# Kernel tuning notes

Hardware: AMD Instinct MI355X
Metric: run time of the kernel (lower is better)

## Reference

```python
import jax, jax.numpy as jnp
import numpy as np

NHEAD = 8
TOPKS = (16, 8, 8)


def _to_tokens(x, nhead):
    # [b,c,h,w] -> [b, h*w, nhead, c//nhead]  (matches 'b c h w -> b (h w) c' then head split)
    b, c, h, w = x.shape
    return x.reshape(b, c, h * w).transpose(0, 2, 1).reshape(b, h * w, nhead, c // nhead)


def _gather_heads(table, idx):
    # table [b,S,nh,d], idx [b,L,K,nh] -> [b,L,K,nh,d]; per-head gather along S
    def per_b(tb, ib):
        return jax.vmap(lambda th, ih: th[ih], in_axes=(1, -1), out_axes=-2)(tb, ib)
    return jax.vmap(per_b)(table, idx)


def _coarse_level(q, k, v, topk, nhead):
    b, c, h, w = k.shape
    d = c // nhead
    qt, kt, vt = _to_tokens(q, nhead), _to_tokens(k, nhead), _to_tokens(v, nhead)
    QK = jnp.einsum('blhd,bshd->blsh', qt, kt) * (d ** -0.5)
    A = jax.nn.softmax(QK, axis=-2)  # softmax over source positions s
    _, ids = jax.lax.top_k(jnp.moveaxis(A, -2, -1), topk)  # top-k over s
    topk_idx = jnp.moveaxis(ids, -1, -2)  # [b, L, topk, nh]
    msg = jnp.einsum('blsh,bshd->blhd', A, vt)
    return msg, topk_idx


def _fine_level(q, k, v, topk_pos, topk_prev, topk, nhead):
    b, c, h0, w0 = q.shape
    _, _, h1, w1 = k.shape
    d = c // nhead
    kt, vt = _to_tokens(k, nhead), _to_tokens(v, nhead)
    # group queries into 2x2 quadrants: [b, (h0/2*w0/2), 4, nh, d]
    qg = q.reshape(b, c, h0 // 2, 2, w0 // 2, 2)
    qg = qg.transpose(0, 2, 4, 3, 5, 1).reshape(b, (h0 // 2) * (w0 // 2), 4, nhead, d)
    py, px = topk_pos[0] * 2, topk_pos[1] * 2  # [b, L, topk_prev, nh]
    # expand each coarse winner into its 4 children at this level
    idx = jnp.stack([(py + x) * w1 + (px + y) for x in (0, 1) for y in (0, 1)], axis=3)
    K = topk_prev * 4
    idx = idx.reshape(b, -1, K, nhead)  # [b, L, K, nh]
    gk = _gather_heads(kt, idx)  # [b, L, K, nh, d]  (score_computation_op gather)
    gv = _gather_heads(vt, idx)  # (value_aggregation_op gather)
    QK = jnp.einsum('blthd,blkhd->bltkh', qg, gk) * (d ** -0.5)
    A = jax.nn.softmax(QK, axis=-2)  # softmax over the K gathered keys
    _, ids = jax.lax.top_k(jnp.moveaxis(A, -2, -1), topk)
    tk_ids = jnp.moveaxis(ids, -1, -2)  # [b, L, 4, topk, nh]
    msg = jnp.einsum('bltkh,blkhd->blthd', A, gv)  # [b, L, 4, nh, d]
    idx_rep = jnp.broadcast_to(idx[:, :, None, :, :], A.shape)
    topk_idx = jnp.take_along_axis(idx_rep, tk_ids, axis=3)  # absolute source positions
    # 'b (h w) (t1 t2) k nh -> b (h t1 w t2) k nh'
    topk_idx = topk_idx.reshape(b, h0 // 2, w0 // 2, 2, 2, topk, nhead)
    topk_idx = topk_idx.transpose(0, 1, 3, 2, 4, 5, 6).reshape(b, h0 * w0, topk, nhead)
    return msg, topk_idx


def _forward(queries, keys, values, weight, nhead=NHEAD, topks=TOPKS):
    messages = []
    topk = topks[0]
    topk_pos = None
    for i, (q, k, v) in enumerate(zip(queries[::-1], keys[::-1], values[::-1])):
        w = k.shape[3]
        if i == 0:
            msg, topk_idx = _coarse_level(q, k, v, topk, nhead)
        else:
            topk_prev, topk = topk, topks[i]
            msg, topk_idx = _fine_level(q, k, v, topk_pos, topk_prev, topk, nhead)
        messages.append(msg)
        topk_pos = (topk_idx // w, topk_idx % w)
    wgt = jax.nn.softmax(weight)
    fm = messages[0] * wgt[0]  # [b, HW_coarse, nh, d]
    for i in range(1, len(messages)):
        fm = fm[:, :, None] + messages[i] * wgt[i]  # [b, L, 4, nh, d]
        H = queries[-i].shape[2]
        b, L, _, nh, d = fm.shape
        W = L // H
        # 'b (H W) (t1 t2) h d -> b (H t1 W t2) h d'
        fm = fm.reshape(b, H, W, 2, 2, nh, d).transpose(0, 1, 3, 2, 4, 5, 6).reshape(b, L * 4, nh, d)
    return fm


def setup_inputs() -> dict:
    key = jax.random.key(0)
    ks = jax.random.split(key, 10)
    B, C = 4, 128
    shapes = [(B, C, 128, 128), (B, C, 64, 64), (B, C, 32, 32)]
    names = ['q0', 'q1', 'q2', 'k0', 'k1', 'k2', 'v0', 'v1', 'v2']
    inp = {}
    for j, n in enumerate(names):
        inp[n] = jax.random.normal(ks[j], shapes[j % 3], dtype=jnp.float32)
    inp['weight'] = jax.random.normal(ks[9], (3,), dtype=jnp.float32)
    return inp


def reference(q0, q1, q2, k0, k1, k2, v0, v1, v2, weight):
    return _forward([q0, q1, q2], [k0, k1, k2], [v0, v1, v2], weight)
```

## Files before the change

kernel.cpp:

```cpp
#include <hip/hip_runtime.h>


#define DEV static __device__ __forceinline__

DEV float wave_max(float v){
  #pragma unroll
  for(int o=32;o>0;o>>=1) v = fmaxf(v, __shfl_xor(v,o,64));
  return v;
}
DEV float wave_sum(float v){
  #pragma unroll
  for(int o=32;o>0;o>>=1) v += __shfl_xor(v,o,64);
  return v;
}
DEV float half_max(float v){
  #pragma unroll
  for(int o=16;o>0;o>>=1) v = fmaxf(v, __shfl_xor(v,o,64));
  return v;
}
DEV float half_sum(float v){
  #pragma unroll
  for(int o=16;o>0;o>>=1) v += __shfl_xor(v,o,64);
  return v;
}
DEV void wave_argmax(float& v, int& idx){
  #pragma unroll
  for(int o=32;o>0;o>>=1){
    float ov = __shfl_xor(v,o,64);
    int   oi = __shfl_xor(idx,o,64);
    if (ov > v || (ov == v && oi < idx)) { v = ov; idx = oi; }
  }
}

DEV void scan4(const float (&sc)[16], unsigned &rem, float (&tv)[4], int (&tc)[4]){
  #pragma unroll
  for(int t=0;t<4;t++){
    float bv=-1e30f; int bc=0;
    #pragma unroll
    for(int c=0;c<16;c++){
      const bool ok = (((rem>>c)&1u)==0u) && (sc[c] > bv);
      bv = ok ? sc[c] : bv;
      bc = ok ? c : bc;
    }
    tv[t]=bv; tc[t]=bc; rem |= (1u<<bc);
  }
}

DEV void top16_pair(const float (&sc0)[16], const float (&sc1)[16], int lane,
                    int &cap0, int &cap1){
  unsigned rem0=0u, rem1=0u;
  float tv0[4], tv1[4]; int tc0[4], tc1[4];
  scan4(sc0, rem0, tv0, tc0);
  scan4(sc1, rem1, tv1, tc1);
  cap0=0; cap1=0;
  #pragma unroll 1
  for(int r=0;r<16;r++){
    const float M0 = wave_max(tv0[0]);
    const float M1 = wave_max(tv1[0]);
    const unsigned long long k0 = __ballot(tv0[0]==M0);
    const unsigned long long k1 = __ballot(tv1[0]==M1);
    int wl0 = (int)__ffsll(k0)-1, ws0;
    int wl1 = (int)__ffsll(k1)-1, ws1;
    if (__popcll(k0)==1){ ws0 = __shfl(tc0[0], wl0)*64 + wl0; }
    else {
      int sel = (tv0[0]==M0) ? (tc0[0]*64+lane) : 0x7fffffff;
      #pragma unroll
      for(int o=32;o>0;o>>=1) sel = min(sel, __shfl_xor(sel,o,64));
      ws0 = sel; wl0 = ws0 & 63;
    }
    if (__popcll(k1)==1){ ws1 = __shfl(tc1[0], wl1)*64 + wl1; }
    else {
      int sel = (tv1[0]==M1) ? (tc1[0]*64+lane) : 0x7fffffff;
      #pragma unroll
      for(int o=32;o>0;o>>=1) sel = min(sel, __shfl_xor(sel,o,64));
      ws1 = sel; wl1 = ws1 & 63;
    }
    cap0 = (lane==r) ? ws0 : cap0;
    cap1 = (lane==r) ? ws1 : cap1;
    if (lane==wl0){
      tv0[0]=tv0[1]; tc0[0]=tc0[1];
      tv0[1]=tv0[2]; tc0[1]=tc0[2];
      tv0[2]=tv0[3]; tc0[2]=tc0[3];
      tv0[3]=-1e30f; tc0[3]=0;
      if (tv0[0] < -1e29f) scan4(sc0, rem0, tv0, tc0);
    }
    if (lane==wl1){
      tv1[0]=tv1[1]; tc1[0]=tc1[1];
      tv1[1]=tv1[2]; tc1[1]=tc1[2];
      tv1[2]=tv1[3]; tc1[2]=tc1[3];
      tv1[3]=-1e30f; tc1[3]=0;
      if (tv1[0] < -1e29f) scan4(sc1, rem1, tv1, tc1);
    }
  }
}

__global__ __launch_bounds__(256) void k_transpose_all(
    const float* __restrict__ k0, const float* __restrict__ v0,
    const float* __restrict__ k1, const float* __restrict__ v1,
    const float* __restrict__ k2, const float* __restrict__ v2,
    float* __restrict__ ktok0, float* __restrict__ vtok0,
    float* __restrict__ ktok1, float* __restrict__ vtok1,
    float* __restrict__ ktok2, float* __restrict__ vtok2)
{
  const int blk = blockIdx.x;
  const float* src; float* dst; int lgS, base;
  if (blk < 4096){ lgS=14; if (blk<2048){src=k0;dst=ktok0;base=0;} else {src=v0;dst=vtok0;base=2048;} }
  else if (blk < 5120){ lgS=12; if (blk<4608){src=k1;dst=ktok1;base=4096;} else {src=v1;dst=vtok1;base=4608;} }
  else { lgS=10; if (blk<5248){src=k2;dst=ktok2;base=5120;} else {src=v2;dst=vtok2;base=5248;} }
  const int id = (blk-base)*256 + threadIdx.x;
  const int s = id & ((1<<lgS)-1), bh = id >> lgS;
  const float* sp = src + ((size_t)bh<<(lgS+4)) + s;
  float r[16];
  #pragma unroll
  for(int dd=0;dd<16;dd++) r[dd] = sp[(size_t)dd<<lgS];
  float4* dp = (float4*)(dst + (size_t)id*16);
  dp[0] = make_float4(r[0],r[1],r[2],r[3]);
  dp[1] = make_float4(r[4],r[5],r[6],r[7]);
  dp[2] = make_float4(r[8],r[9],r[10],r[11]);
  dp[3] = make_float4(r[12],r[13],r[14],r[15]);
}

template<bool TOK>
__global__ __launch_bounds__(256) void k_coarse(
    const float* __restrict__ q, const float* __restrict__ k, const float* __restrict__ v,
    const float* __restrict__ ktok, const float* __restrict__ vtok,
    float* __restrict__ msg0, int* __restrict__ topk0)
{
  const int tid = threadIdx.x, wid = tid>>6, lane = tid&63;
  const int gq0 = __builtin_amdgcn_readfirstlane((blockIdx.x*4 + wid)*2);
  const int bh = gq0>>10, l0 = gq0&1023;

  const float* qb = q + (size_t)bh*16384;
  float qv0[16], qv1[16];
  #pragma unroll
  for(int dd=0;dd<16;dd++){ qv0[dd]=qb[dd*1024+l0]; qv1[dd]=qb[dd*1024+l0+1]; }

  float sc0[16], sc1[16];
  #pragma unroll
  for(int c=0;c<16;c++){
    const int s = c*64 + lane;
    float kr[16];
    if constexpr (TOK){
      const float4* kp = (const float4*)(ktok + ((size_t)bh*1024 + s)*16);
      float4 x0=kp[0], x1=kp[1], x2=kp[2], x3=kp[3];
      kr[0]=x0.x; kr[1]=x0.y; kr[2]=x0.z; kr[3]=x0.w;
      kr[4]=x1.x; kr[5]=x1.y; kr[6]=x1.z; kr[7]=x1.w;
      kr[8]=x2.x; kr[9]=x2.y; kr[10]=x2.z; kr[11]=x2.w;
      kr[12]=x3.x; kr[13]=x3.y; kr[14]=x3.z; kr[15]=x3.w;
    } else {
      const float* kb = k + (size_t)bh*16384 + s;
      #pragma unroll
      for(int dd=0;dd<16;dd++) kr[dd] = kb[dd*1024];
    }
    float a0=0.f, a1=0.f;
    #pragma unroll
    for(int dd=0;dd<16;dd++){ a0=fmaf(qv0[dd],kr[dd],a0); a1=fmaf(qv1[dd],kr[dd],a1); }
    sc0[c]=a0*0.25f; sc1[c]=a1*0.25f;
  }

  int cap0, cap1;
  top16_pair(sc0, sc1, lane, cap0, cap1);
  if (lane < 16){
    topk0[(size_t)gq0*16 + lane]     = cap0;
    topk0[(size_t)(gq0+1)*16 + lane] = cap1;
  }

  float m0=-1e30f, m1=-1e30f;
  #pragma unroll
  for(int c=0;c<16;c++){ m0=fmaxf(m0,sc0[c]); m1=fmaxf(m1,sc1[c]); }
  m0 = wave_max(m0); m1 = wave_max(m1);
  float s0=0.f, s1=0.f;
  #pragma unroll
  for(int c=0;c<16;c++){ sc0[c]=__expf(sc0[c]-m0); sc1[c]=__expf(sc1[c]-m1); s0+=sc0[c]; s1+=sc1[c]; }
  s0 = wave_sum(s0); s1 = wave_sum(s1);
  const float i0=1.0f/s0, i1=1.0f/s1;
  #pragma unroll
  for(int c=0;c<16;c++){ sc0[c]*=i0; sc1[c]*=i1; }

  float acc0[16], acc1[16];
  #pragma unroll
  for(int dd=0;dd<16;dd++){ acc0[dd]=0.f; acc1[dd]=0.f; }
  #pragma unroll
  for(int c=0;c<16;c++){
    const int s = c*64 + lane;
    float vr[16];
    if constexpr (TOK){
      const float4* vp = (const float4*)(vtok + ((size_t)bh*1024 + s)*16);
      float4 x0=vp[0], x1=vp[1], x2=vp[2], x3=vp[3];
      vr[0]=x0.x; vr[1]=x0.y; vr[2]=x0.z; vr[3]=x0.w;
      vr[4]=x1.x; vr[5]=x1.y; vr[6]=x1.z; vr[7]=x1.w;
      vr[8]=x2.x; vr[9]=x2.y; vr[10]=x2.z; vr[11]=x2.w;
      vr[12]=x3.x; vr[13]=x3.y; vr[14]=x3.z; vr[15]=x3.w;
    } else {
      const float* vb = v + (size_t)bh*16384 + s;
      #pragma unroll
      for(int dd=0;dd<16;dd++) vr[dd] = vb[dd*1024];
    }
    const float p0c = sc0[c], p1c = sc1[c];
    #pragma unroll
    for(int dd=0;dd<16;dd++){ acc0[dd]=fmaf(p0c,vr[dd],acc0[dd]); acc1[dd]=fmaf(p1c,vr[dd],acc1[dd]); }
  }
  #pragma unroll
  for(int dd=0;dd<16;dd++){ acc0[dd]=wave_sum(acc0[dd]); acc1[dd]=wave_sum(acc1[dd]); }
  {
    float val = 0.f;
    #pragma unroll
    for(int dd=0;dd<16;dd++){
      val = (lane==dd)    ? acc0[dd] : val;
      val = (lane==16+dd) ? acc1[dd] : val;
    }
    if (lane < 32) msg0[(size_t)(gq0 + (lane>>4))*16 + (lane&15)] = val;
  }
}

template<bool TOK>
__global__ __launch_bounds__(256) void k_mid(
    const float* __restrict__ q, const float* __restrict__ k, const float* __restrict__ v,
    const float* __restrict__ ktok, const float* __restrict__ vtok,
    const int* __restrict__ topk0, float* __restrict__ msg1, int* __restrict__ topk1)
{
  __shared__ float s_v[4][16][66];
  __shared__ float s_e[4][4][65];
  __shared__ float s_k[TOK?1:4][16][66];
  const int tid = threadIdx.x, wid = tid>>6, lane = tid&63;
  const int slot = __builtin_amdgcn_readfirstlane(blockIdx.x*4 + wid);
  const int l = slot & 1023, bh = slot >> 10;
  const int gy = l>>5, gx = l&31;
  const float* qb = q + (size_t)bh*65536;

  float kv[16];
  if constexpr (TOK){
    const int w = lane>>2, c = lane&3;
    const int widx = topk0[(size_t)slot*16 + w];
    const int pos = (2*(widx>>5) + (c>>1))*64 + 2*(widx&31) + (c&1);
    const float4* kp = (const float4*)(ktok + ((size_t)bh*4096 + pos)*16);
    float4 x0=kp[0], x1=kp[1], x2=kp[2], x3=kp[3];
    kv[0]=x0.x; kv[1]=x0.y; kv[2]=x0.z; kv[3]=x0.w;
    kv[4]=x1.x; kv[5]=x1.y; kv[6]=x1.z; kv[7]=x1.w;
    kv[8]=x2.x; kv[9]=x2.y; kv[10]=x2.z; kv[11]=x2.w;
    kv[12]=x3.x; kv[13]=x3.y; kv[14]=x3.z; kv[15]=x3.w;
    const float4* vp = (const float4*)(vtok + ((size_t)bh*4096 + pos)*16);
    float4 y0=vp[0], y1=vp[1], y2=vp[2], y3=vp[3];
    s_v[wid][0][lane]=y0.x;  s_v[wid][1][lane]=y0.y;  s_v[wid][2][lane]=y0.z;  s_v[wid][3][lane]=y0.w;
    s_v[wid][4][lane]=y1.x;  s_v[wid][5][lane]=y1.y;  s_v[wid][6][lane]=y1.z;  s_v[wid][7][lane]=y1.w;
    s_v[wid][8][lane]=y2.x;  s_v[wid][9][lane]=y2.y;  s_v[wid][10][lane]=y2.z; s_v[wid][11][lane]=y2.w;
    s_v[wid][12][lane]=y3.x; s_v[wid][13][lane]=y3.y; s_v[wid][14][lane]=y3.z; s_v[wid][15][lane]=y3.w;
  } else {
    const int kvsel = lane>>5, rr = lane&31, w = rr>>1, cy = rr&1;
    const int widx = topk0[(size_t)slot*16 + w];
    const int base = (2*(widx>>5) + cy)*64 + 2*(widx&31);
    const float* src = (kvsel ? v : k) + (size_t)bh*65536;
    float* dst = kvsel ? &s_v[wid][0][0] : &s_k[wid][0][0];
    const int key0 = w*4 + cy*2;
    #pragma unroll
    for(int dd=0;dd<16;dd++){
      const float2 f2 = *(const float2*)(src + dd*4096 + base);
      *(float2*)(dst + dd*66 + key0) = f2;
    }
    #pragma unroll
    for(int dd=0;dd<16;dd++) kv[dd] = s_k[wid][dd][lane];
  }

  #pragma unroll
  for(int t=0;t<4;t++){
    const int qp = (2*gy + (t>>1))*64 + 2*gx + (t&1);
    float a = 0.f;
    #pragma unroll
    for(int dd=0;dd<16;dd++) a = fmaf(qb[dd*4096 + qp], kv[dd], a);
    a *= 0.25f;
    const float m = wave_max(a);
    const float e = __expf(a - m);
    const float s = wave_sum(e);
    s_e[wid][t][lane] = e / s;
  }

  const int g = lane>>4, j = lane&15;
  {
    const int wj_ = topk0[(size_t)slot*16 + j];
    const int tyj = wj_>>5, txj = wj_&31;
    int posj[4];
    #pragma unroll
    for(int e=0;e<4;e++) posj[e] = (2*tyj + (e>>1))*64 + 2*txj + (e&1);
    float ev[4];
    #pragma unroll
    for(int e=0;e<4;e++) ev[e] = s_e[wid][g][j*4+e];
    int cap = 0;
    for(int r=0;r<8;r++){
      float lv = ev[0]; int le = 0;
      #pragma unroll
      for(int e=1;e<4;e++) if (ev[e] > lv){ lv=ev[e]; le=e; }
      float gv = lv; int gk = j*4 + le;
      #pragma unroll
      for(int o=8;o>0;o>>=1){
        float ov = __shfl_xor(gv,o,64); int ok = __shfl_xor(gk,o,64);
        if (ov > gv || (ov == gv && ok < gk)){ gv=ov; gk=ok; }
      }
      const int estar = gk&3, h = gk>>2;
      int seli = posj[0];
      seli = (estar==1) ? posj[1] : seli;
      seli = (estar==2) ? posj[2] : seli;
      seli = (estar==3) ? posj[3] : seli;
      const int wpos = __shfl(seli, (lane & 48) | h, 64);
      #pragma unroll
      for(int e=0;e<4;e++) if (j==h && e==estar) ev[e] = -1e30f;
      if (j == r) cap = wpos;
    }
    if (j < 8){
      const int sp = (2*gy + (g>>1))*64 + 2*gx + (g&1);
      topk1[((size_t)bh*4096 + sp)*8 + j] = cap;
    }
  }

  {
    const int t = lane>>4, dd = lane&15;
    float a = 0.f;
    #pragma unroll
    for(int kk=0;kk<64;kk++) a = fmaf(s_e[wid][t][kk], s_v[wid][dd][kk], a);
    const int sp = (2*gy + (t>>1))*64 + 2*gx + (t&1);
    msg1[((size_t)bh*4096 + sp)*16 + dd] = a;
  }
}

template<bool TOK>
__global__ __launch_bounds__(256) void k_fine(
    const float* __restrict__ q, const float* __restrict__ k, const float* __restrict__ v,
    const float* __restrict__ ktok, const float* __restrict__ vtok,
    const int* __restrict__ topk1, const float* __restrict__ msg0,
    const float* __restrict__ msg1, const float* __restrict__ wvec,
    float* __restrict__ out)
{
  __shared__ float s_k[4][16][34];
  __shared__ float s_v[4][16][34];
  __shared__ float s_q[4][4][17];
  __shared__ float s_e[4][4][33];
  const int tid = threadIdx.x, wid = tid>>6, lane = tid&63;
  const int slot = __builtin_amdgcn_readfirstlane(blockIdx.x*4 + wid);
  const int l = slot & 4095, bh = slot >> 12;
  const int b = bh>>3, h = bh&7;
  const int gy = l>>6, gx = l&63;

  const float* qb = q + (size_t)bh*262144;

  {
    const int t = lane>>4, dd = lane&15;
    const int qp = (2*gy + (t>>1))*128 + 2*gx + (t&1);
    s_q[wid][t][dd] = qb[dd*16384 + qp];
  }
  if constexpr (TOK){
    const int key = lane&31, half = lane>>5;
    const int w = key>>2, c = key&3;
    const int widx = topk1[(size_t)slot*8 + w];
    const int pos = (2*(widx>>6) + (c>>1))*128 + 2*(widx&63) + (c&1);
    const float4* sp4 = (const float4*)((half ? vtok : ktok) + ((size_t)bh*16384 + pos)*16);
    float4 x0=sp4[0], x1=sp4[1], x2=sp4[2], x3=sp4[3];
    float* dst = (half ? &s_v[wid][0][0] : &s_k[wid][0][0]);
    dst[0*34+key]=x0.x;  dst[1*34+key]=x0.y;  dst[2*34+key]=x0.z;  dst[3*34+key]=x0.w;
    dst[4*34+key]=x1.x;  dst[5*34+key]=x1.y;  dst[6*34+key]=x1.z;  dst[7*34+key]=x1.w;
    dst[8*34+key]=x2.x;  dst[9*34+key]=x2.y;  dst[10*34+key]=x2.z; dst[11*34+key]=x2.w;
    dst[12*34+key]=x3.x; dst[13*34+key]=x3.y; dst[14*34+key]=x3.z; dst[15*34+key]=x3.w;
  } else {
    const int gs = lane>>1, dh = lane&1;
    const int kvsel = gs>>4, rr = gs&15, w = rr>>1, cy = rr&1;
    const int widx = topk1[(size_t)slot*8 + w];
    const int base = (2*(widx>>6) + cy)*128 + 2*(widx&63);
    const float* src = (kvsel ? v : k) + (size_t)bh*262144;
    float* dst = kvsel ? &s_v[wid][0][0] : &s_k[wid][0][0];
    const int key0 = w*4 + cy*2;
    #pragma unroll
    for(int jj=0;jj<8;jj++){
      const int dd = dh*8 + jj;
      const float2 f2 = *(const float2*)(src + dd*16384 + base);
      *(float2*)(dst + dd*34 + key0) = f2;
    }
  }

  const int key = lane&31, th = lane>>5;
  float kv[16];
  #pragma unroll
  for(int dd=0;dd<16;dd++) kv[dd] = s_k[wid][dd][key];
  #pragma unroll
  for(int tt=0;tt<2;tt++){
    const int t = th*2 + tt;
    float a = 0.f;
    #pragma unroll
    for(int dd=0;dd<16;dd++) a = fmaf(s_q[wid][t][dd], kv[dd], a);
    a *= 0.25f;
    const float m = half_max(a);
    const float e = __expf(a - m);
    const float s = half_sum(e);
    s_e[wid][t][key] = e / s;
  }

  const float w0i = wvec[0], w1i = wvec[1], w2i = wvec[2];
  const float wm = fmaxf(w0i, fmaxf(w1i, w2i));
  float e0 = __expf(w0i-wm), e1 = __expf(w1i-wm), e2 = __expf(w2i-wm);
  const float wsum = e0+e1+e2;
  e0/=wsum; e1/=wsum; e2/=wsum;

  const int t2 = lane>>4, dd2 = lane&15;
  float a = 0.f;
  #pragma unroll
  for(int kk=0;kk<32;kk++) a = fmaf(s_e[wid][t2][kk], s_v[wid][dd2][kk], a);

  const int cl = (gy>>1)*32 + (gx>>1);
  const float m0 = msg0[((size_t)bh*1024 + cl)*16 + dd2];
  const float m1 = msg1[(size_t)slot*16 + dd2];
  const int pp = (2*gy + (t2>>1))*128 + 2*gx + (t2&1);
  out[(((size_t)b*16384 + pp)*8 + h)*16 + dd2] = e0*m0 + e1*m1 + e2*a;
}

extern "C" void kernel_launch(void* const* d_in, const int* in_sizes, int n_in,
                              void* d_out, int out_size, void* d_ws, size_t ws_size,
                              hipStream_t stream) {
  const float* q0 = (const float*)d_in[0];
  const float* q1 = (const float*)d_in[1];
  const float* q2 = (const float*)d_in[2];
  const float* k0 = (const float*)d_in[3];
  const float* k1 = (const float*)d_in[4];
  const float* k2 = (const float*)d_in[5];
  const float* v0 = (const float*)d_in[6];
  const float* v1 = (const float*)d_in[7];
  const float* v2 = (const float*)d_in[8];
  const float* wv = (const float*)d_in[9];
  float* out = (float*)d_out;

  float* msg0  = (float*)d_ws;
  int*   topk0 = (int*)(msg0 + 524288);
  float* msg1  = (float*)(topk0 + 524288);
  int*   topk1 = (int*)(msg1 + 2097152);
  float* ktok0 = (float*)(topk1 + 1048576);
  float* vtok0 = ktok0 + 8388608;
  float* ktok1 = vtok0 + 8388608;
  float* vtok1 = ktok1 + 2097152;
  float* ktok2 = vtok1 + 2097152;
  float* vtok2 = ktok2 + 524288;

  const size_t needA = (size_t)(4194304 + 22020096) * 4;
  const size_t needB = (size_t)(4194304 + 16777216) * 4;
  const bool tA = ws_size >= needA;
  const bool tB = ws_size >= needB;

  if (tA){
    hipLaunchKernelGGL(k_transpose_all, dim3(5376), dim3(256), 0, stream,
                       k0,v0,k1,v1,k2,v2, ktok0,vtok0,ktok1,vtok1,ktok2,vtok2);
    hipLaunchKernelGGL(k_coarse<true>, dim3(4096),  dim3(256), 0, stream, q2,k2,v2, ktok2,vtok2, msg0, topk0);
    hipLaunchKernelGGL(k_mid<true>,    dim3(8192),  dim3(256), 0, stream, q1,k1,v1, ktok1,vtok1, topk0, msg1, topk1);
    hipLaunchKernelGGL(k_fine<true>,   dim3(32768), dim3(256), 0, stream, q0,k0,v0, ktok0,vtok0, topk1, msg0, msg1, wv, out);
  } else if (tB){
    hipLaunchKernelGGL(k_transpose_all, dim3(4096), dim3(256), 0, stream,
                       k0,v0,k0,v0,k0,v0, ktok0,vtok0,ktok0,vtok0,ktok0,vtok0);
    hipLaunchKernelGGL(k_coarse<false>, dim3(4096),  dim3(256), 0, stream, q2,k2,v2, ktok0,vtok0, msg0, topk0);
    hipLaunchKernelGGL(k_mid<false>,    dim3(8192),  dim3(256), 0, stream, q1,k1,v1, ktok0,vtok0, topk0, msg1, topk1);
    hipLaunchKernelGGL(k_fine<true>,    dim3(32768), dim3(256), 0, stream, q0,k0,v0, ktok0,vtok0, topk1, msg0, msg1, wv, out);
  } else {
    hipLaunchKernelGGL(k_coarse<false>, dim3(4096),  dim3(256), 0, stream, q2,k2,v2, (float*)d_ws,(float*)d_ws, msg0, topk0);
    hipLaunchKernelGGL(k_mid<false>,    dim3(8192),  dim3(256), 0, stream, q1,k1,v1, (float*)d_ws,(float*)d_ws, topk0, msg1, topk1);
    hipLaunchKernelGGL(k_fine<false>,   dim3(32768), dim3(256), 0, stream, q0,k0,v0, (float*)d_ws,(float*)d_ws, topk1, msg0, msg1, wv, out);
  }
}
```

Measured before the change: 463.8 us.

## Stage coarse K/V via shared memory and pre-transpose queries for mid/fine levels

The coarse kernel no longer uses pre-transposed K/V. Each block now cooperatively loads channel-major K and V chunks into shared memory as float4 and reuses them across four waves, with a new score-index mapping so top-k indices stay correct. The transpose kernel drops the level-2 K/V and adds level-0 and level-1 query transposes, so the mid and fine kernels read contiguous token-major Q rows when the workspace is large enough. This trades the strided Q gathers and the level-2 transpose for extra transpose traffic on Q and block-level syncs in the coarse kernel.

Result: slower. 521.9 us (+12.5%).

```diff
diff --git a/kernel.cpp b/kernel.cpp
--- a/kernel.cpp
+++ b/kernel.cpp
@@ -31,6 +31,8 @@
     if (ov > v || (ov == v && oi < idx)) { v = ov; idx = oi; }
   }
 }
+
+DEV int s_of(int j, int lane){ return ((j>>2)<<8) + lane*4 + (j&3); }
 
 DEV void scan4(const float (&sc)[16], unsigned &rem, float (&tv)[4], int (&tc)[4]){
   #pragma unroll
@@ -61,52 +63,63 @@
     const unsigned long long k1 = __ballot(tv1[0]==M1);
     int wl0 = (int)__ffsll(k0)-1, ws0;
     int wl1 = (int)__ffsll(k1)-1, ws1;
-    if (__popcll(k0)==1){ ws0 = __shfl(tc0[0], wl0)*64 + wl0; }
+    if (__popcll(k0)==1){ const int jw = __shfl(tc0[0], wl0); ws0 = s_of(jw, wl0); }
     else {
-      int sel = (tv0[0]==M0) ? (tc0[0]*64+lane) : 0x7fffffff;
+      int sel = (tv0[0]==M0) ? s_of(tc0[0], lane) : 0x7fffffff;
       #pragma unroll
       for(int o=32;o>0;o>>=1) sel = min(sel, __shfl_xor(sel,o,64));
-      ws0 = sel; wl0 = ws0 & 63;
-    }
-    if (__popcll(k1)==1){ ws1 = __shfl(tc1[0], wl1)*64 + wl1; }
+      ws0 = sel; wl0 = (ws0>>2)&63;
+    }
+    if (__popcll(k1)==1){ const int jw = __shfl(tc1[0], wl1); ws1 = s_of(jw, wl1); }
     else {
-      int sel = (tv1[0]==M1) ? (tc1[0]*64+lane) : 0x7fffffff;
+      int sel = (tv1[0]==M1) ? s_of(tc1[0], lane) : 0x7fffffff;
       #pragma unroll
       for(int o=32;o>0;o>>=1) sel = min(sel, __shfl_xor(sel,o,64));
-      ws1 = sel; wl1 = ws1 & 63;
+      ws1 = sel; wl1 = (ws1>>2)&63;
     }
     cap0 = (lane==r) ? ws0 : cap0;
     cap1 = (lane==r) ? ws1 : cap1;
     if (lane==wl0){
+      const int jw = ((ws0>>8)<<2) | (ws0&3);
       tv0[0]=tv0[1]; tc0[0]=tc0[1];
       tv0[1]=tv0[2]; tc0[1]=tc0[2];
       tv0[2]=tv0[3]; tc0[2]=tc0[3];
-      tv0[3]=-1e30f; tc0[3]=0;
+      tv0[3]=-1e30f; tc0[3]=jw*0;
       if (tv0[0] < -1e29f) scan4(sc0, rem0, tv0, tc0);
     }
     if (lane==wl1){
+      const int jw = ((ws1>>8)<<2) | (ws1&3);
       tv1[0]=tv1[1]; tc1[0]=tc1[1];
       tv1[1]=tv1[2]; tc1[1]=tc1[2];
       tv1[2]=tv1[3]; tc1[2]=tc1[3];
-      tv1[3]=-1e30f; tc1[3]=0;
+      tv1[3]=-1e30f; tc1[3]=jw*0;
       if (tv1[0] < -1e29f) scan4(sc1, rem1, tv1, tc1);
     }
   }
 }
 
+template<bool HASQ>
 __global__ __launch_bounds__(256) void k_transpose_all(
-    const float* __restrict__ k0, const float* __restrict__ v0,
-    const float* __restrict__ k1, const float* __restrict__ v1,
-    const float* __restrict__ k2, const float* __restrict__ v2,
-    float* __restrict__ ktok0, float* __restrict__ vtok0,
-    float* __restrict__ ktok1, float* __restrict__ vtok1,
-    float* __restrict__ ktok2, float* __restrict__ vtok2)
+    const float* __restrict__ k0, const float* __restrict__ v0, const float* __restrict__ q0,
+    const float* __restrict__ k1, const float* __restrict__ v1, const float* __restrict__ q1,
+    float* __restrict__ ktok0, float* __restrict__ vtok0, float* __restrict__ qtok0,
+    float* __restrict__ ktok1, float* __restrict__ vtok1, float* __restrict__ qtok1)
 {
   const int blk = blockIdx.x;
   const float* src; float* dst; int lgS, base;
-  if (blk < 4096){ lgS=14; if (blk<2048){src=k0;dst=ktok0;base=0;} else {src=v0;dst=vtok0;base=2048;} }
-  else if (blk < 5120){ lgS=12; if (blk<4608){src=k1;dst=ktok1;base=4096;} else {src=v1;dst=vtok1;base=4608;} }
-  else { lgS=10; if (blk<5248){src=k2;dst=ktok2;base=5120;} else {src=v2;dst=vtok2;base=5248;} }
+  if (HASQ){
+    if      (blk < 2048){ lgS=14; src=k0; dst=ktok0; base=0; }
+    else if (blk < 4096){ lgS=14; src=v0; dst=vtok0; base=2048; }
+    else if (blk < 6144){ lgS=14; src=q0; dst=qtok0; base=4096; }
+    else if (blk < 6656){ lgS=12; src=k1; dst=ktok1; base=6144; }
+    else if (blk < 7168){ lgS=12; src=v1; dst=vtok1; base=6656; }
+    else                { lgS=12; src=q1; dst=qtok1; base=7168; }
+  } else {
+    if      (blk < 2048){ lgS=14; src=k0; dst=ktok0; base=0; }
+    else if (blk < 4096){ lgS=14; src=v0; dst=vtok0; base=2048; }
+    else if (blk < 4608){ lgS=12; src=k1; dst=ktok1; base=4096; }
+    else                { lgS=12; src=v1; dst=vtok1; base=4608; }
+  }
   const int id = (blk-base)*256 + threadIdx.x;
   const int s = id & ((1<<lgS)-1), bh = id >> lgS;
   const float* sp = src + ((size_t)bh<<(lgS+4)) + s;
@@ -120,43 +133,49 @@
   dp[3] = make_float4(r[12],r[13],r[14],r[15]);
 }
 
-template<bool TOK>
 __global__ __launch_bounds__(256) void k_coarse(
     const float* __restrict__ q, const float* __restrict__ k, const float* __restrict__ v,
-    const float* __restrict__ ktok, const float* __restrict__ vtok,
     float* __restrict__ msg0, int* __restrict__ topk0)
 {
+  __shared__ float4 s_t[16*64];
   const int tid = threadIdx.x, wid = tid>>6, lane = tid&63;
-  const int gq0 = __builtin_amdgcn_readfirstlane((blockIdx.x*4 + wid)*2);
-  const int bh = gq0>>10, l0 = gq0&1023;
+  const int blk = blockIdx.x;
+  const int bh  = blk>>7;
+  const int l0  = (blk&127)*8 + wid*2;
+  const int gq0 = bh*1024 + l0;
 
   const float* qb = q + (size_t)bh*16384;
+  const float* kb = k + (size_t)bh*16384;
+  const float* vb = v + (size_t)bh*16384;
+
   float qv0[16], qv1[16];
   #pragma unroll
   for(int dd=0;dd<16;dd++){ qv0[dd]=qb[dd*1024+l0]; qv1[dd]=qb[dd*1024+l0+1]; }
 
   float sc0[16], sc1[16];
   #pragma unroll
-  for(int c=0;c<16;c++){
-    const int s = c*64 + lane;
-    float kr[16];
-    if constexpr (TOK){
-      const float4* kp = (const float4*)(ktok + ((size_t)bh*1024 + s)*16);
-      float4 x0=kp[0], x1=kp[1], x2=kp[2], x3=kp[3];
-      kr[0]=x0.x; kr[1]=x0.y; kr[2]=x0.z; kr[3]=x0.w;
-      kr[4]=x1.x; kr[5]=x1.y; kr[6]=x1.z; kr[7]=x1.w;
-      kr[8]=x2.x; kr[9]=x2.y; kr[10]=x2.z; kr[11]=x2.w;
-      kr[12]=x3.x; kr[13]=x3.y; kr[14]=x3.z; kr[15]=x3.w;
-    } else {
-      const float* kb = k + (size_t)bh*16384 + s;
-      #pragma unroll
-      for(int dd=0;dd<16;dd++) kr[dd] = kb[dd*1024];
-    }
-    float a0=0.f, a1=0.f;
-    #pragma unroll
-    for(int dd=0;dd<16;dd++){ a0=fmaf(qv0[dd],kr[dd],a0); a1=fmaf(qv1[dd],kr[dd],a1); }
-    sc0[c]=a0*0.25f; sc1[c]=a1*0.25f;
-  }
+  for(int j=0;j<16;j++){ sc0[j]=0.f; sc1[j]=0.f; }
+  #pragma unroll
+  for(int ch=0;ch<4;ch++){
+    __syncthreads();
+    #pragma unroll
+    for(int i=0;i<4;i++){
+      const int f = tid + i*256, dd = f>>6, g = f&63;
+      s_t[f] = ((const float4*)(kb + dd*1024 + ch*256))[g];
+    }
+    __syncthreads();
+    #pragma unroll
+    for(int dd=0;dd<16;dd++){
+      const float4 kf = s_t[dd*64 + lane];
+      const float q0d = qv0[dd], q1d = qv1[dd];
+      sc0[ch*4+0]=fmaf(q0d,kf.x,sc0[ch*4+0]); sc0[ch*4+1]=fmaf(q0d,kf.y,sc0[ch*4+1]);
+      sc0[ch*4+2]=fmaf(q0d,kf.z,sc0[ch*4+2]); sc0[ch*4+3]=fmaf(q0d,kf.w,sc0[ch*4+3]);
+      sc1[ch*4+0]=fmaf(q1d,kf.x,sc1[ch*4+0]); sc1[ch*4+1]=fmaf(q1d,kf.y,sc1[ch*4+1]);
+      sc1[ch*4+2]=fmaf(q1d,kf.z,sc1[ch*4+2]); sc1[ch*4+3]=fmaf(q1d,kf.w,sc1[ch*4+3]);
+    }
+  }
+  #pragma unroll
+  for(int j=0;j<16;j++){ sc0[j]*=0.25f; sc1[j]*=0.25f; }
 
   int cap0, cap1;
   top16_pair(sc0, sc1, lane, cap0, cap1);
@@ -167,38 +186,36 @@
 
   float m0=-1e30f, m1=-1e30f;
   #pragma unroll
-  for(int c=0;c<16;c++){ m0=fmaxf(m0,sc0[c]); m1=fmaxf(m1,sc1[c]); }
+  for(int j=0;j<16;j++){ m0=fmaxf(m0,sc0[j]); m1=fmaxf(m1,sc1[j]); }
   m0 = wave_max(m0); m1 = wave_max(m1);
   float s0=0.f, s1=0.f;
   #pragma unroll
-  for(int c=0;c<16;c++){ sc0[c]=__expf(sc0[c]-m0); sc1[c]=__expf(sc1[c]-m1); s0+=sc0[c]; s1+=sc1[c]; }
+  for(int j=0;j<16;j++){ sc0[j]=__expf(sc0[j]-m0); sc1[j]=__expf(sc1[j]-m1); s0+=sc0[j]; s1+=sc1[j]; }
   s0 = wave_sum(s0); s1 = wave_sum(s1);
   const float i0=1.0f/s0, i1=1.0f/s1;
   #pragma unroll
-  for(int c=0;c<16;c++){ sc0[c]*=i0; sc1[c]*=i1; }
+  for(int j=0;j<16;j++){ sc0[j]*=i0; sc1[j]*=i1; }
 
   float acc0[16], acc1[16];
   #pragma unroll
   for(int dd=0;dd<16;dd++){ acc0[dd]=0.f; acc1[dd]=0.f; }
   #pragma unroll
-  for(int c=0;c<16;c++){
-    const int s = c*64 + lane;
-    float vr[16];
-    if constexpr (TOK){
-      const float4* vp = (const float4*)(vtok + ((size_t)bh*1024 + s)*16);
-      float4 x0=vp[0], x1=vp[1], x2=vp[2], x3=vp[3];
-      vr[0]=x0.x; vr[1]=x0.y; vr[2]=x0.z; vr[3]=x0.w;
-      vr[4]=x1.x; vr[5]=x1.y; vr[6]=x1.z; vr[7]=x1.w;
-      vr[8]=x2.x; vr[9]=x2.y; vr[10]=x2.z; vr[11]=x2.w;
-      vr[12]=x3.x; vr[13]=x3.y; vr[14]=x3.z; vr[15]=x3.w;
-    } else {
-      const float* vb = v + (size_t)bh*16384 + s;
-      #pragma unroll
-      for(int dd=0;dd<16;dd++) vr[dd] = vb[dd*1024];
-    }
-    const float p0c = sc0[c], p1c = sc1[c];
-    #pragma unroll
-    for(int dd=0;dd<16;dd++){ acc0[dd]=fmaf(p0c,vr[dd],acc0[dd]); acc1[dd]=fmaf(p1c,vr[dd],acc1[dd]); }
+  for(int ch=0;ch<4;ch++){
+    __syncthreads();
+    #pragma unroll
+    for(int i=0;i<4;i++){
+      const int f = tid + i*256, dd = f>>6, g = f&63;
+      s_t[f] = ((const float4*)(vb + dd*1024 + ch*256))[g];
+    }
+    __syncthreads();
+    #pragma unroll
+    for(int dd=0;dd<16;dd++){
+      const float4 vf = s_t[dd*64 + lane];
+      acc0[dd]=fmaf(sc0[ch*4+0],vf.x,acc0[dd]); acc0[dd]=fmaf(sc0[ch*4+1],vf.y,acc0[dd]);
+      acc0[dd]=fmaf(sc0[ch*4+2],vf.z,acc0[dd]); acc0[dd]=fmaf(sc0[ch*4+3],vf.w,acc0[dd]);
+      acc1[dd]=fmaf(sc1[ch*4+0],vf.x,acc1[dd]); acc1[dd]=fmaf(sc1[ch*4+1],vf.y,acc1[dd]);
+      acc1[dd]=fmaf(sc1[ch*4+2],vf.z,acc1[dd]); acc1[dd]=fmaf(sc1[ch*4+3],vf.w,acc1[dd]);
+    }
   }
   #pragma unroll
   for(int dd=0;dd<16;dd++){ acc0[dd]=wave_sum(acc0[dd]); acc1[dd]=wave_sum(acc1[dd]); }
@@ -213,10 +230,11 @@
   }
 }
 
-template<bool TOK>
+template<bool TOK, bool TOKQ>
 __global__ __launch_bounds__(256) void k_mid(
     const float* __restrict__ q, const float* __restrict__ k, const float* __restrict__ v,
     const float* __restrict__ ktok, const float* __restrict__ vtok,
+    const float* __restrict__ qtok,
     const int* __restrict__ topk0, float* __restrict__ msg1, int* __restrict__ topk1)
 {
   __shared__ float s_v[4][16][66];
@@ -265,8 +283,14 @@
   for(int t=0;t<4;t++){
     const int qp = (2*gy + (t>>1))*64 + 2*gx + (t&1);
     float a = 0.f;
-    #pragma unroll
-    for(int dd=0;dd<16;dd++) a = fmaf(qb[dd*4096 + qp], kv[dd], a);
+    if constexpr (TOKQ){
+      const float* qr = qtok + ((size_t)bh*4096 + qp)*16;
+      #pragma unroll
+      for(int dd=0;dd<16;dd++) a = fmaf(qr[dd], kv[dd], a);
+    } else {
+      #pragma unroll
+      for(int dd=0;dd<16;dd++) a = fmaf(qb[dd*4096 + qp], kv[dd], a);
+    }
     a *= 0.25f;
     const float m = wave_max(a);
     const float e = __expf(a - m);
@@ -321,10 +345,11 @@
   }
 }
 
-template<bool TOK>
+template<bool TOK, bool TOKQ>
 __global__ __launch_bounds__(256) void k_fine(
     const float* __restrict__ q, const float* __restrict__ k, const float* __restrict__ v,
     const float* __restrict__ ktok, const float* __restrict__ vtok,
+    const float* __restrict__ qtok,
     const int* __restrict__ topk1, const float* __restrict__ msg0,
     const float* __restrict__ msg1, const float* __restrict__ wvec,
     float* __restrict__ out)
@@ -341,7 +366,15 @@
 
   const float* qb = q + (size_t)bh*262144;
 
-  {
+  if constexpr (TOKQ){
+    if (lane < 16){
+      const int t = lane>>2, f4 = lane&3;
+      const int qp = (2*gy + (t>>1))*128 + 2*gx + (t&1);
+      const float4 x = ((const float4*)(qtok + ((size_t)bh*16384 + qp)*16))[f4];
+      s_q[wid][t][f4*4+0]=x.x; s_q[wid][t][f4*4+1]=x.y;
+      s_q[wid][t][f4*4+2]=x.z; s_q[wid][t][f4*4+3]=x.w;
+    }
+  } else {
     const int t = lane>>4, dd = lane&15;
     const int qp = (2*gy + (t>>1))*128 + 2*gx + (t&1);
     s_q[wid][t][dd] = qb[dd*16384 + qp];
@@ -432,29 +465,32 @@
   float* vtok0 = ktok0 + 8388608;
   float* ktok1 = vtok0 + 8388608;
   float* vtok1 = ktok1 + 2097152;
-  float* ktok2 = vtok1 + 2097152;
-  float* vtok2 = ktok2 + 524288;
-
-  const size_t needA = (size_t)(4194304 + 22020096) * 4;
-  const size_t needB = (size_t)(4194304 + 16777216) * 4;
-  const bool tA = ws_size >= needA;
-  const bool tB = ws_size >= needB;
-
-  if (tA){
-    hipLaunchKernelGGL(k_transpose_all, dim3(5376), dim3(256), 0, stream,
-                       k0,v0,k1,v1,k2,v2, ktok0,vtok0,ktok1,vtok1,ktok2,vtok2);
-    hipLaunchKernelGGL(k_coarse<true>, dim3(4096),  dim3(256), 0, stream, q2,k2,v2, ktok2,vtok2, msg0, topk0);
-    hipLaunchKernelGGL(k_mid<true>,    dim3(8192),  dim3(256), 0, stream, q1,k1,v1, ktok1,vtok1, topk0, msg1, topk1);
-    hipLaunchKernelGGL(k_fine<true>,   dim3(32768), dim3(256), 0, stream, q0,k0,v0, ktok0,vtok0, topk1, msg0, msg1, wv, out);
-  } else if (tB){
-    hipLaunchKernelGGL(k_transpose_all, dim3(4096), dim3(256), 0, stream,
-                       k0,v0,k0,v0,k0,v0, ktok0,vtok0,ktok0,vtok0,ktok0,vtok0);
-    hipLaunchKernelGGL(k_coarse<false>, dim3(4096),  dim3(256), 0, stream, q2,k2,v2, ktok0,vtok0, msg0, topk0);
-    hipLaunchKernelGGL(k_mid<false>,    dim3(8192),  dim3(256), 0, stream, q1,k1,v1, ktok0,vtok0, topk0, msg1, topk1);
-    hipLaunchKernelGGL(k_fine<true>,    dim3(32768), dim3(256), 0, stream, q0,k0,v0, ktok0,vtok0, topk1, msg0, msg1, wv, out);
+  float* qtok0 = vtok1 + 2097152;
+  float* qtok1 = qtok0 + 8388608;
+
+  const size_t needC = (size_t)(4194304 + 31457280) * 4;
+  const size_t needA = (size_t)(4194304 + 20971520) * 4;
+
+  hipLaunchKernelGGL(k_coarse, dim3(4096), dim3(256), 0, stream, q2, k2, v2, msg0, topk0);
+
+  if (ws_size >= needC){
+    hipLaunchKernelGGL(k_transpose_all<true>, dim3(7680), dim3(256), 0, stream,
+                       k0,v0,q0,k1,v1,q1, ktok0,vtok0,qtok0,ktok1,vtok1,qtok1);
+    hipLaunchKernelGGL((k_mid<true,true>),  dim3(8192),  dim3(256), 0, stream,
+                       q1,k1,v1, ktok1,vtok1,qtok1, topk0, msg1, topk1);
+    hipLaunchKernelGGL((k_fine<true,true>), dim3(32768), dim3(256), 0, stream,
+                       q0,k0,v0, ktok0,vtok0,qtok0, topk1, msg0, msg1, wv, out);
+  } else if (ws_size >= needA){
+    hipLaunchKernelGGL(k_transpose_all<false>, dim3(5120), dim3(256), 0, stream,
+                       k0,v0,q0,k1,v1,q1, ktok0,vtok0,qtok0,ktok1,vtok1,qtok1);
+    hipLaunchKernelGGL((k_mid<true,false>),  dim3(8192),  dim3(256), 0, stream,
+                       q1,k1,v1, ktok1,vtok1,qtok1, topk0, msg1, topk1);
+    hipLaunchKernelGGL((k_fine<true,false>), dim3(32768), dim3(256), 0, stream,
+                       q0,k0,v0, ktok0,vtok0,qtok0, topk1, msg0, msg1, wv, out);
   } else {
-    hipLaunchKernelGGL(k_coarse<false>, dim3(4096),  dim3(256), 0, stream, q2,k2,v2, (float*)d_ws,(float*)d_ws, msg0, topk0);
-    hipLaunchKernelGGL(k_mid<false>,    dim3(8192),  dim3(256), 0, stream, q1,k1,v1, (float*)d_ws,(float*)d_ws, topk0, msg1, topk1);
-    hipLaunchKernelGGL(k_fine<false>,   dim3(32768), dim3(256), 0, stream, q0,k0,v0, (float*)d_ws,(float*)d_ws, topk1, msg0, msg1, wv, out);
-  }
-}
+    hipLaunchKernelGGL((k_mid<false,false>),  dim3(8192),  dim3(256), 0, stream,
+                       q1,k1,v1, (float*)d_ws,(float*)d_ws,(float*)d_ws, topk0, msg1, topk1);
+    hipLaunchKernelGGL((k_fine<false,false>), dim3(32768), dim3(256), 0, stream,
+                       q0,k0,v0, (float*)d_ws,(float*)d_ws,(float*)d_ws, topk1, msg0, msg1, wv, out);
+  }
+}
```

## Overlap coarse attention with level-0/1 transposes in one interleaved kernel

Applied to the files above, without the earlier changes.

Splits the k2/v2 transpose into a small pre-kernel, then launches one combined kernel whose even blocks run the coarse attention level while odd blocks transpose the large level-0/1 K/V tensors into token-major layout. The compute-bound coarse work can then overlap the bandwidth-bound transposes instead of running after them. It also prescales q by the softmax scale, merges the two per-query max/sum reductions into one shuffle chain, and folds the 16-channel output reduction with a butterfly that defers normalization. The middle workspace fallback path is removed, and block-type divergence inside the combined kernel may cost some occupancy.

Result: slower. 586.4 us (+26.5%).

```diff
diff --git a/kernel.cpp b/kernel.cpp
--- a/kernel.cpp
+++ b/kernel.cpp
@@ -94,46 +94,36 @@
   }
 }
 
-__global__ __launch_bounds__(256) void k_transpose_all(
-    const float* __restrict__ k0, const float* __restrict__ v0,
-    const float* __restrict__ k1, const float* __restrict__ v1,
-    const float* __restrict__ k2, const float* __restrict__ v2,
-    float* __restrict__ ktok0, float* __restrict__ vtok0,
-    float* __restrict__ ktok1, float* __restrict__ vtok1,
-    float* __restrict__ ktok2, float* __restrict__ vtok2)
-{
-  const int blk = blockIdx.x;
-  const float* src; float* dst; int lgS, base;
-  if (blk < 4096){ lgS=14; if (blk<2048){src=k0;dst=ktok0;base=0;} else {src=v0;dst=vtok0;base=2048;} }
-  else if (blk < 5120){ lgS=12; if (blk<4608){src=k1;dst=ktok1;base=4096;} else {src=v1;dst=vtok1;base=4608;} }
-  else { lgS=10; if (blk<5248){src=k2;dst=ktok2;base=5120;} else {src=v2;dst=vtok2;base=5248;} }
-  const int id = (blk-base)*256 + threadIdx.x;
-  const int s = id & ((1<<lgS)-1), bh = id >> lgS;
-  const float* sp = src + ((size_t)bh<<(lgS+4)) + s;
-  float r[16];
-  #pragma unroll
-  for(int dd=0;dd<16;dd++) r[dd] = sp[(size_t)dd<<lgS];
-  float4* dp = (float4*)(dst + (size_t)id*16);
-  dp[0] = make_float4(r[0],r[1],r[2],r[3]);
-  dp[1] = make_float4(r[4],r[5],r[6],r[7]);
-  dp[2] = make_float4(r[8],r[9],r[10],r[11]);
-  dp[3] = make_float4(r[12],r[13],r[14],r[15]);
+DEV float fold16(float (&a)[16], int lane){
+  #pragma unroll
+  for(int st=0; st<4; st++){
+    const int o = 1<<st, nh = 8>>st;
+    const int b = (lane>>st)&1;
+    #pragma unroll
+    for(int i=0;i<nh;i++){
+      const float x = a[2*i], y = a[2*i+1];
+      const float send = b ? x : y;
+      const float keep = b ? y : x;
+      a[i] = keep + __shfl_xor(send, o, 64);
+    }
+  }
+  return a[0];
 }
 
 template<bool TOK>
-__global__ __launch_bounds__(256) void k_coarse(
+DEV void coarse_block(int cid, int tid,
     const float* __restrict__ q, const float* __restrict__ k, const float* __restrict__ v,
     const float* __restrict__ ktok, const float* __restrict__ vtok,
     float* __restrict__ msg0, int* __restrict__ topk0)
 {
-  const int tid = threadIdx.x, wid = tid>>6, lane = tid&63;
-  const int gq0 = __builtin_amdgcn_readfirstlane((blockIdx.x*4 + wid)*2);
+  const int wid = tid>>6, lane = tid&63;
+  const int gq0 = __builtin_amdgcn_readfirstlane((cid*4 + wid)*2);
   const int bh = gq0>>10, l0 = gq0&1023;
 
   const float* qb = q + (size_t)bh*16384;
   float qv0[16], qv1[16];
   #pragma unroll
-  for(int dd=0;dd<16;dd++){ qv0[dd]=qb[dd*1024+l0]; qv1[dd]=qb[dd*1024+l0+1]; }
+  for(int dd=0;dd<16;dd++){ qv0[dd]=qb[dd*1024+l0]*0.25f; qv1[dd]=qb[dd*1024+l0+1]*0.25f; }
 
   float sc0[16], sc1[16];
   #pragma unroll
@@ -155,7 +145,7 @@
     float a0=0.f, a1=0.f;
     #pragma unroll
     for(int dd=0;dd<16;dd++){ a0=fmaf(qv0[dd],kr[dd],a0); a1=fmaf(qv1[dd],kr[dd],a1); }
-    sc0[c]=a0*0.25f; sc1[c]=a1*0.25f;
+    sc0[c]=a0; sc1[c]=a1;
   }
 
   int cap0, cap1;
@@ -165,17 +155,42 @@
     topk0[(size_t)(gq0+1)*16 + lane] = cap1;
   }
 
-  float m0=-1e30f, m1=-1e30f;
-  #pragma unroll
-  for(int c=0;c<16;c++){ m0=fmaxf(m0,sc0[c]); m1=fmaxf(m1,sc1[c]); }
-  m0 = wave_max(m0); m1 = wave_max(m1);
-  float s0=0.f, s1=0.f;
-  #pragma unroll
-  for(int c=0;c<16;c++){ sc0[c]=__expf(sc0[c]-m0); sc1[c]=__expf(sc1[c]-m1); s0+=sc0[c]; s1+=sc1[c]; }
-  s0 = wave_sum(s0); s1 = wave_sum(s1);
-  const float i0=1.0f/s0, i1=1.0f/s1;
-  #pragma unroll
-  for(int c=0;c<16;c++){ sc0[c]*=i0; sc1[c]*=i1; }
+  float m0l=-1e30f, m1l=-1e30f;
+  #pragma unroll
+  for(int c=0;c<16;c++){ m0l=fmaxf(m0l,sc0[c]); m1l=fmaxf(m1l,sc1[c]); }
+  float m0, m1;
+  {
+    float t  = (lane&16) ? m1l : m0l;
+    float sd = (lane&16) ? m0l : m1l;
+    t = fmaxf(t, __shfl_xor(sd,16,64));
+    t = fmaxf(t, __shfl_xor(t,32,64));
+    t = fmaxf(t, __shfl_xor(t, 8,64));
+    t = fmaxf(t, __shfl_xor(t, 4,64));
+    t = fmaxf(t, __shfl_xor(t, 2,64));
+    t = fmaxf(t, __shfl_xor(t, 1,64));
+    const float to = __shfl_xor(t,16,64);
+    m0 = (lane&16) ? to : t;
+    m1 = (lane&16) ? t  : to;
+  }
+
+  float s0l=0.f, s1l=0.f;
+  #pragma unroll
+  for(int c=0;c<16;c++){
+    sc0[c]=__expf(sc0[c]-m0); s0l+=sc0[c];
+    sc1[c]=__expf(sc1[c]-m1); s1l+=sc1[c];
+  }
+  float inv;
+  {
+    float t  = (lane&16) ? s1l : s0l;
+    float sd = (lane&16) ? s0l : s1l;
+    t += __shfl_xor(sd,16,64);
+    t += __shfl_xor(t,32,64);
+    t += __shfl_xor(t, 8,64);
+    t += __shfl_xor(t, 4,64);
+    t += __shfl_xor(t, 2,64);
+    t += __shfl_xor(t, 1,64);
+    inv = 1.0f / t;
+  }
 
   float acc0[16], acc1[16];
   #pragma unroll
@@ -200,17 +215,82 @@
     #pragma unroll
     for(int dd=0;dd<16;dd++){ acc0[dd]=fmaf(p0c,vr[dd],acc0[dd]); acc1[dd]=fmaf(p1c,vr[dd],acc1[dd]); }
   }
-  #pragma unroll
-  for(int dd=0;dd<16;dd++){ acc0[dd]=wave_sum(acc0[dd]); acc1[dd]=wave_sum(acc1[dd]); }
+
+  const float a0f = fold16(acc0, lane);
+  const float a1f = fold16(acc1, lane);
   {
-    float val = 0.f;
-    #pragma unroll
-    for(int dd=0;dd<16;dd++){
-      val = (lane==dd)    ? acc0[dd] : val;
-      val = (lane==16+dd) ? acc1[dd] : val;
-    }
-    if (lane < 32) msg0[(size_t)(gq0 + (lane>>4))*16 + (lane&15)] = val;
-  }
+    const float mine = (lane&16) ? a1f : a0f;
+    const float send = (lane&16) ? a0f : a1f;
+    float tot = mine + __shfl_xor(send,16,64);
+    tot += __shfl_xor(tot,32,64);
+    tot *= inv;
+    if (lane < 32) msg0[(size_t)(gq0 + (lane>>4))*16 + (lane&15)] = tot;
+  }
+}
+
+__global__ __launch_bounds__(256) void k_pre(
+    const float* __restrict__ k2, const float* __restrict__ v2,
+    float* __restrict__ ktok2, float* __restrict__ vtok2)
+{
+  const int blk = blockIdx.x;
+  const float* src = (blk<128) ? k2 : v2;
+  float* dst = (blk<128) ? ktok2 : vtok2;
+  const int id = (blk & 127)*256 + threadIdx.x;
+  const int s = id & 1023, bh = id >> 10;
+  const float* sp = src + ((size_t)bh<<14) + s;
+  float r[16];
+  #pragma unroll
+  for(int dd=0;dd<16;dd++) r[dd] = sp[(size_t)dd<<10];
+  float4* dp = (float4*)(dst + (size_t)id*16);
+  dp[0] = make_float4(r[0],r[1],r[2],r[3]);
+  dp[1] = make_float4(r[4],r[5],r[6],r[7]);
+  dp[2] = make_float4(r[8],r[9],r[10],r[11]);
+  dp[3] = make_float4(r[12],r[13],r[14],r[15]);
+}
+
+__global__ __launch_bounds__(256) void k_mega(
+    const float* __restrict__ q2, const float* __restrict__ k2, const float* __restrict__ v2,
+    const float* __restrict__ ktok2, const float* __restrict__ vtok2,
+    float* __restrict__ msg0, int* __restrict__ topk0,
+    const float* __restrict__ k0, const float* __restrict__ v0,
+    const float* __restrict__ k1, const float* __restrict__ v1,
+    float* __restrict__ ktok0, float* __restrict__ vtok0,
+    float* __restrict__ ktok1, float* __restrict__ vtok1)
+{
+  const int idx = blockIdx.x;
+  int tb;
+  if (idx < 8192){
+    if ((idx & 1) == 0){
+      coarse_block<true>(idx>>1, threadIdx.x, q2,k2,v2, ktok2,vtok2, msg0, topk0);
+      return;
+    }
+    tb = idx>>1;
+  } else {
+    tb = 4096 + (idx - 8192);
+  }
+  const float* src; float* dst; int lgS, base;
+  if      (tb < 2048){ lgS=14; src=k0; dst=ktok0; base=0; }
+  else if (tb < 4096){ lgS=14; src=v0; dst=vtok0; base=2048; }
+  else if (tb < 4608){ lgS=12; src=k1; dst=ktok1; base=4096; }
+  else               { lgS=12; src=v1; dst=vtok1; base=4608; }
+  const int id = (tb-base)*256 + threadIdx.x;
+  const int s = id & ((1<<lgS)-1), bh = id >> lgS;
+  const float* sp = src + ((size_t)bh<<(lgS+4)) + s;
+  float r[16];
+  #pragma unroll
+  for(int dd=0;dd<16;dd++) r[dd] = sp[(size_t)dd<<lgS];
+  float4* dp = (float4*)(dst + (size_t)id*16);
+  dp[0] = make_float4(r[0],r[1],r[2],r[3]);
+  dp[1] = make_float4(r[4],r[5],r[6],r[7]);
+  dp[2] = make_float4(r[8],r[9],r[10],r[11]);
+  dp[3] = make_float4(r[12],r[13],r[14],r[15]);
+}
+
+__global__ __launch_bounds__(256) void k_coarse_fb(
+    const float* __restrict__ q, const float* __restrict__ k, const float* __restrict__ v,
+    float* __restrict__ msg0, int* __restrict__ topk0)
+{
+  coarse_block<false>(blockIdx.x, threadIdx.x, q,k,v, nullptr,nullptr, msg0, topk0);
 }
 
 template<bool TOK>
@@ -436,25 +516,21 @@
   float* vtok2 = ktok2 + 524288;
 
   const size_t needA = (size_t)(4194304 + 22020096) * 4;
-  const size_t needB = (size_t)(4194304 + 16777216) * 4;
-  const bool tA = ws_size >= needA;
-  const bool tB = ws_size >= needB;
-
-  if (tA){
-    hipLaunchKernelGGL(k_transpose_all, dim3(5376), dim3(256), 0, stream,
-                       k0,v0,k1,v1,k2,v2, ktok0,vtok0,ktok1,vtok1,ktok2,vtok2);
-    hipLaunchKernelGGL(k_coarse<true>, dim3(4096),  dim3(256), 0, stream, q2,k2,v2, ktok2,vtok2, msg0, topk0);
-    hipLaunchKernelGGL(k_mid<true>,    dim3(8192),  dim3(256), 0, stream, q1,k1,v1, ktok1,vtok1, topk0, msg1, topk1);
-    hipLaunchKernelGGL(k_fine<true>,   dim3(32768), dim3(256), 0, stream, q0,k0,v0, ktok0,vtok0, topk1, msg0, msg1, wv, out);
-  } else if (tB){
-    hipLaunchKernelGGL(k_transpose_all, dim3(4096), dim3(256), 0, stream,
-                       k0,v0,k0,v0,k0,v0, ktok0,vtok0,ktok0,vtok0,ktok0,vtok0);
-    hipLaunchKernelGGL(k_coarse<false>, dim3(4096),  dim3(256), 0, stream, q2,k2,v2, ktok0,vtok0, msg0, topk0);
-    hipLaunchKernelGGL(k_mid<false>,    dim3(8192),  dim3(256), 0, stream, q1,k1,v1, ktok0,vtok0, topk0, msg1, topk1);
-    hipLaunchKernelGGL(k_fine<true>,    dim3(32768), dim3(256), 0, stream, q0,k0,v0, ktok0,vtok0, topk1, msg0, msg1, wv, out);
+
+  if (ws_size >= needA){
+    hipLaunchKernelGGL(k_pre,  dim3(256),  dim3(256), 0, stream, k2, v2, ktok2, vtok2);
+    hipLaunchKernelGGL(k_mega, dim3(9216), dim3(256), 0, stream,
+                       q2,k2,v2, ktok2,vtok2, msg0, topk0,
+                       k0,v0,k1,v1, ktok0,vtok0,ktok1,vtok1);
+    hipLaunchKernelGGL(k_mid<true>,  dim3(8192),  dim3(256), 0, stream,
+                       q1,k1,v1, ktok1,vtok1, topk0, msg1, topk1);
+    hipLaunchKernelGGL(k_fine<true>, dim3(32768), dim3(256), 0, stream,
+                       q0,k0,v0, ktok0,vtok0, topk1, msg0, msg1, wv, out);
   } else {
-    hipLaunchKernelGGL(k_coarse<false>, dim3(4096),  dim3(256), 0, stream, q2,k2,v2, (float*)d_ws,(float*)d_ws, msg0, topk0);
-    hipLaunchKernelGGL(k_mid<false>,    dim3(8192),  dim3(256), 0, stream, q1,k1,v1, (float*)d_ws,(float*)d_ws, topk0, msg1, topk1);
-    hipLaunchKernelGGL(k_fine<false>,   dim3(32768), dim3(256), 0, stream, q0,k0,v0, (float*)d_ws,(float*)d_ws, topk1, msg0, msg1, wv, out);
-  }
-}
+    hipLaunchKernelGGL(k_coarse_fb,   dim3(4096),  dim3(256), 0, stream, q2,k2,v2, msg0, topk0);
+    hipLaunchKernelGGL(k_mid<false>,  dim3(8192),  dim3(256), 0, stream,
+                       q1,k1,v1, (float*)d_ws,(float*)d_ws, topk0, msg1, topk1);
+    hipLaunchKernelGGL(k_fine<false>, dim3(32768), dim3(256), 0, stream,
+                       q0,k0,v0, (float*)d_ws,(float*)d_ws, topk1, msg0, msg1, wv, out);
+  }
+}
```
